# Kernel tuning notes

Measured on AMD Instinct MI355X. Metric: run time of the kernel, lower is better.

The kernel has to match this reference:

```python
import jax, jax.numpy as jnp
import numpy as np

TOP_K = 2
LORA_SCALE = 32.0 / 16.0  # alpha / r


def setup_inputs() -> dict:
    key = jax.random.key(0)
    ks = jax.random.split(key, 11)
    B, S, D, F, E, R = 4, 1024, 2048, 5632, 8, 16
    sd, sf = 1.0 / np.sqrt(D), 1.0 / np.sqrt(F)
    return {
        "x": jax.random.normal(ks[0], (B, S, D), jnp.float32),
        "gate_w": jax.random.normal(ks[1], (E, D), jnp.float32) * 0.02,
        "w1": jax.random.normal(ks[2], (F, D), jnp.float32) * sd,
        "w3": jax.random.normal(ks[3], (F, D), jnp.float32) * sd,
        "w2": jax.random.normal(ks[4], (D, F), jnp.float32) * sf,
        "a1": jax.random.normal(ks[5], (E, R, D), jnp.float32) * sd,
        "b1": jax.random.normal(ks[6], (E, F, R), jnp.float32) * 0.01,
        "a3": jax.random.normal(ks[7], (E, R, D), jnp.float32) * sd,
        "b3": jax.random.normal(ks[8], (E, F, R), jnp.float32) * 0.01,
        "a2": jax.random.normal(ks[9], (E, R, F), jnp.float32) * sf,
        "b2": jax.random.normal(ks[10], (E, D, R), jnp.float32) * 0.01,
    }


def reference(x, gate_w, w1, w3, w2, a1, b1, a3, b3, a2, b2):
    B, S, D = x.shape
    E = gate_w.shape[0]
    xf = x.reshape(B * S, D)                      # [N, D] tokens
    N = xf.shape[0]

    # Mixtral-style router: top-k over expert logits, softmax over selected.
    logits = xf @ gate_w.T                        # [N, E]
    top_w, top_i = jax.lax.top_k(logits, TOP_K)   # [N, k]
    routing = jax.nn.softmax(top_w, axis=-1)
    # Dense [N, E] routing-weight matrix (zero for unselected experts).
    w_full = jnp.zeros((N, E), x.dtype).at[jnp.arange(N)[:, None], top_i].add(routing)

    # Shared base up-projections computed once (same for every expert).
    base1 = xf @ w1.T                             # [N, F]
    base3 = xf @ w3.T                             # [N, F]

    def expert_step(acc, p):
        A1, B1, A3, B3, A2, B2, we = p            # we: [N] routing weight
        h1 = base1 + ((xf @ A1.T) @ B1.T) * LORA_SCALE
        h3 = base3 + ((xf @ A3.T) @ B3.T) * LORA_SCALE
        act = jax.nn.silu(h1) * h3                # SwiGLU, per-expert
        out = act @ w2.T + ((act @ A2.T) @ B2.T) * LORA_SCALE
        return acc + we[:, None] * out, None

    init = jnp.zeros((N, D), x.dtype)
    out, _ = jax.lax.scan(expert_step, init, (a1, b1, a3, b3, a2, b2, w_full.T))
    return out.reshape(B, S, D)
```

## Files before the change

### kernel.cpp

```cpp
#include <hip/hip_runtime.h>
#include <stdint.h>

#define NTOK 4096
#define DDIM 2048
#define FDIM 5632
#define NEXP 8
#define RLORA 16
#define TWOF 11264
#define BCOLS 11520
#define PADROWS 10240
#define LSCALE 2.0f

typedef __attribute__((ext_vector_type(4))) float f32x4;
typedef __attribute__((ext_vector_type(8))) short short8;
typedef unsigned short u16;

#define AS1 __attribute__((address_space(1)))
#define AS3 __attribute__((address_space(3)))

__device__ __forceinline__ float b2f(short s) {
  union { float f; unsigned u; } v;
  v.u = ((unsigned)(u16)s) << 16;
  return v.f;
}
__device__ __forceinline__ u16 f2b(float f) {
  union { float f; unsigned u; } v; v.f = f;
  unsigned r = v.u + 0x7fffu + ((v.u >> 16) & 1u);
  return (u16)(r >> 16);
}

__global__ __launch_bounds__(256) void cast_kernel(const float* __restrict__ src, u16* __restrict__ dst, int n4) {
  int stride = gridDim.x * 256;
  for (int i = blockIdx.x * 256 + threadIdx.x; i < n4; i += stride) {
    float4 v = reinterpret_cast<const float4*>(src)[i];
    ushort4 o;
    o.x = f2b(v.x); o.y = f2b(v.y); o.z = f2b(v.z); o.w = f2b(v.w);
    reinterpret_cast<ushort4*>(dst)[i] = o;
  }
}

__global__ __launch_bounds__(256) void cast_ball(const float* __restrict__ w1, const float* __restrict__ w3,
                                                 const float* __restrict__ a1, const float* __restrict__ a3,
                                                 u16* __restrict__ Ball) {
  const int n4 = BCOLS * DDIM / 4;
  int stride = gridDim.x * 256;
  for (int i = blockIdx.x * 256 + threadIdx.x; i < n4; i += stride) {
    int row = i >> 9;
    int c4 = i & 511;
    const float* src;
    if (row < FDIM)            src = w1 + (size_t)row * DDIM;
    else if (row < TWOF)       src = w3 + (size_t)(row - FDIM) * DDIM;
    else if (row < TWOF + 128) src = a1 + (size_t)(row - TWOF) * DDIM;
    else                       src = a3 + (size_t)(row - TWOF - 128) * DDIM;
    float4 v = reinterpret_cast<const float4*>(src)[c4];
    ushort4 o;
    o.x = f2b(v.x); o.y = f2b(v.y); o.z = f2b(v.z); o.w = f2b(v.w);
    reinterpret_cast<ushort4*>(Ball)[i] = o;
  }
}

__global__ __launch_bounds__(256) void router_cast(const float* __restrict__ x, const float* __restrict__ gw,
                                                   int2* __restrict__ tok_e, float2* __restrict__ tok_w,
                                                   u16* __restrict__ xb) {
  int tok = blockIdx.x;
  const float* xr = x + (size_t)tok * DDIM;
  int j0 = threadIdx.x * 8;
  float4 v0 = *reinterpret_cast<const float4*>(xr + j0);
  float4 v1 = *reinterpret_cast<const float4*>(xr + j0 + 4);
  float v[8] = {v0.x, v0.y, v0.z, v0.w, v1.x, v1.y, v1.z, v1.w};
  short8 ob;
#pragma unroll
  for (int j = 0; j < 8; ++j) ob[j] = (short)f2b(v[j]);
  *reinterpret_cast<short8*>(xb + (size_t)tok * DDIM + j0) = ob;
  float acc[NEXP];
#pragma unroll
  for (int e = 0; e < NEXP; ++e) {
    const float* gr = gw + e * DDIM + j0;
    float s = 0.f;
#pragma unroll
    for (int j = 0; j < 8; ++j) s += v[j] * gr[j];
    acc[e] = s;
  }
#pragma unroll
  for (int e = 0; e < NEXP; ++e) {
#pragma unroll
    for (int off = 32; off > 0; off >>= 1) acc[e] += __shfl_down(acc[e], off);
  }
  __shared__ float red[4][NEXP];
  int wid = threadIdx.x >> 6;
  int lane = threadIdx.x & 63;
  if (lane == 0) {
#pragma unroll
    for (int e = 0; e < NEXP; ++e) red[wid][e] = acc[e];
  }
  __syncthreads();
  if (threadIdx.x == 0) {
    float l[NEXP];
#pragma unroll
    for (int e = 0; e < NEXP; ++e) l[e] = red[0][e] + red[1][e] + red[2][e] + red[3][e];
    int i0 = 0;
#pragma unroll
    for (int e = 1; e < NEXP; ++e) if (l[e] > l[i0]) i0 = e;
    int i1 = (i0 == 0) ? 1 : 0;
#pragma unroll
    for (int e = 0; e < NEXP; ++e) if (e != i0 && e != i1 && l[e] > l[i1]) i1 = e;
    float ex = __expf(l[i1] - l[i0]);
    float w0 = 1.f / (1.f + ex);
    float w1v = ex / (1.f + ex);
    int2 ev; ev.x = i0; ev.y = i1;
    float2 wv; wv.x = w0; wv.y = w1v;
    tok_e[tok] = ev;
    tok_w[tok] = wv;
  }
}

__global__ __launch_bounds__(256) void build_pairs(const int2* __restrict__ tok_e,
                                                   int* __restrict__ pair_tok,
                                                   int* __restrict__ pair_k, int* __restrict__ poff) {
  __shared__ int cnt[NEXP];
  __shared__ int base[NEXP + 1];
  __shared__ int cur[NEXP];
  if (threadIdx.x < NEXP) cnt[threadIdx.x] = 0;
  __syncthreads();
  for (int t = threadIdx.x; t < NTOK; t += 256) {
    int2 ee = tok_e[t];
    atomicAdd(&cnt[ee.x], 1);
    atomicAdd(&cnt[ee.y], 1);
  }
  for (int i = threadIdx.x; i < PADROWS; i += 256) pair_tok[i] = -1;
  __syncthreads();
  if (threadIdx.x == 0) {
    int o = 0;
#pragma unroll
    for (int e = 0; e < NEXP; ++e) { base[e] = o; o += ((cnt[e] + 255) >> 8) << 8; }
    base[NEXP] = o;
  }
  __syncthreads();
  if (threadIdx.x < NEXP) cur[threadIdx.x] = base[threadIdx.x];
  __syncthreads();
  for (int t = threadIdx.x; t < NTOK; t += 256) {
    int2 ee = tok_e[t];
    int s0 = atomicAdd(&cur[ee.x], 1);
    pair_tok[s0] = t; pair_k[s0] = 0;
    int s1 = atomicAdd(&cur[ee.y], 1);
    pair_tok[s1] = t; pair_k[s1] = 1;
  }
  __syncthreads();
  if (threadIdx.x <= NEXP) poff[threadIdx.x] = base[threadIdx.x];
}

__device__ __forceinline__ void stage64(const u16* __restrict__ src, int ld, char* ldsb, int tid) {
#pragma unroll
  for (int h = 0; h < 4; ++h) {
    int q = h * 256 + tid;
    int r = q >> 3, g = q & 7;
    int gs = g ^ (r & 7);
    const char* s = (const char*)(src + (size_t)r * ld) + gs * 16;
    __builtin_amdgcn_global_load_lds((const AS1 void*)s, (AS3 void*)(ldsb + q * 16), 16, 0, 0);
  }
}

__device__ __forceinline__ void mm128(const u16* __restrict__ A, const u16* __restrict__ B,
                                      int lda, int ldb, int NT,
                                      char* lA, char* lB, int tid,
                                      int rowAb, int rowBb, int col0,
                                      f32x4 (&acc)[4][4]) {
  for (int t = 0; t < NT; ++t) {
    __syncthreads();
    stage64(A + (size_t)t * 64, lda, lA, tid);
    stage64(B + (size_t)t * 64, ldb, lB, tid);
    __syncthreads();
    short8 av[4], bv[4];
#pragma unroll
    for (int kh = 0; kh < 2; ++kh) {
      int col = col0 ^ (kh << 6);
#pragma unroll
      for (int i = 0; i < 4; ++i) {
        av[i] = *(const short8*)(lA + rowAb + i * 2048 + col);
        bv[i] = *(const short8*)(lB + rowBb + i * 2048 + col);
      }
#pragma unroll
      for (int i = 0; i < 4; ++i)
#pragma unroll
        for (int j = 0; j < 4; ++j)
          acc[i][j] = __builtin_amdgcn_mfma_f32_16x16x32_bf16(av[i], bv[j], acc[i][j], 0, 0, 0);
    }
  }
}

__global__ __launch_bounds__(256, 4) void gemm_base(const u16* __restrict__ xb, const u16* __restrict__ Ball,
                                                    u16* __restrict__ base13) {
  __shared__ char lA[16384];
  __shared__ char lB[16384];
  const int tid = threadIdx.x;
  const int lane = tid & 63, wid = tid >> 6;
  const int wr = wid >> 1, wc = wid & 1;
  const int lm = lane & 15, lg = lane >> 4;
  const int col0 = (lg << 4) ^ ((lm & 7) << 4);
  const int rowAb = (wr * 64 + lm) * 128;
  const int rowBb = (wc * 64 + lm) * 128;
  const int lq = (lane >> 4) << 2;
  int orig = blockIdx.x;
  int wgid = (orig & 7) * 360 + (orig >> 3);
  int mi = wgid & 31, nt = wgid >> 5;
  int m0 = mi << 7, n0 = nt << 7;
  f32x4 acc[4][4];
  f32x4 z = {0.f, 0.f, 0.f, 0.f};
#pragma unroll
  for (int i = 0; i < 4; ++i)
#pragma unroll
    for (int j = 0; j < 4; ++j) acc[i][j] = z;
  mm128(xb + (size_t)m0 * DDIM, Ball + (size_t)n0 * DDIM, DDIM, DDIM, DDIM / 64,
        lA, lB, tid, rowAb, rowBb, col0, acc);
#pragma unroll
  for (int i = 0; i < 4; ++i) {
#pragma unroll
    for (int n = 0; n < 4; ++n) {
      int col = n0 + wc * 64 + n * 16 + lm;
#pragma unroll
      for (int q = 0; q < 4; ++q) {
        int row = m0 + wr * 64 + i * 16 + lq + q;
        base13[(size_t)row * BCOLS + col] = f2b(acc[i][n][q]);
      }
    }
  }
}

__global__ __launch_bounds__(256) void act_kernel(const u16* __restrict__ base13,
                                                  const float* __restrict__ b1, const float* __restrict__ b3,
                                                  const int* __restrict__ pair_tok, const int* __restrict__ poff,
                                                  u16* __restrict__ act) {
  __shared__ float lb1[128 * 16];
  __shared__ float lb3[128 * 16];
  int f0 = blockIdx.x * 128;
  int r0 = blockIdx.y * 32;
  if (r0 >= poff[NEXP]) return;
  int e = 0;
  while (r0 >= poff[e + 1]) ++e;
  const float4* pb1 = reinterpret_cast<const float4*>(b1 + ((size_t)e * FDIM + f0) * RLORA);
  const float4* pb3 = reinterpret_cast<const float4*>(b3 + ((size_t)e * FDIM + f0) * RLORA);
  for (int i = threadIdx.x; i < 128 * 16 / 4; i += 256) {
    int r = i >> 2, c = i & 3;
    int cs = (c + (r >> 5)) & 3;
    *reinterpret_cast<float4*>(lb1 + r * 16 + cs * 4) = pb1[i];
    *reinterpret_cast<float4*>(lb3 + r * 16 + cs * 4) = pb3[i];
  }
  __syncthreads();
  int pr = r0 + (threadIdx.x >> 3);
  int fg = (threadIdx.x & 7) << 4;
  int tok = pair_tok[pr];
  if (tok < 0) return;
  const u16* bp = base13 + (size_t)tok * BCOLS;
  short8 x1a = *(const short8*)(bp + TWOF + e * 16);
  short8 x1b = *(const short8*)(bp + TWOF + e * 16 + 8);
  short8 x3a = *(const short8*)(bp + TWOF + NEXP * RLORA + e * 16);
  short8 x3b = *(const short8*)(bp + TWOF + NEXP * RLORA + e * 16 + 8);
  float xa1[16], xa3[16];
#pragma unroll
  for (int r = 0; r < 8; ++r) {
    xa1[r] = b2f(x1a[r]); xa1[r + 8] = b2f(x1b[r]);
    xa3[r] = b2f(x3a[r]); xa3[r + 8] = b2f(x3b[r]);
  }
  short8 h1a = *(const short8*)(bp + f0 + fg);
  short8 h1b = *(const short8*)(bp + f0 + fg + 8);
  short8 h3a = *(const short8*)(bp + FDIM + f0 + fg);
  short8 h3b = *(const short8*)(bp + FDIM + f0 + fg + 8);
  short8 o0, o1;
#pragma unroll
  for (int ii = 0; ii < 16; ++ii) {
    float hb1 = b2f(ii < 8 ? h1a[ii] : h1b[ii - 8]);
    float hb3 = b2f(ii < 8 ? h3a[ii] : h3b[ii - 8]);
    int row = fg + ii;
    int rot = row >> 5;
    const float* l1 = lb1 + row * 16;
    const float* l3 = lb3 + row * 16;
    float d1 = 0.f, d3 = 0.f;
#pragma unroll
    for (int c = 0; c < 4; ++c) {
      int cs = ((c + rot) & 3) << 2;
      float4 v1 = *reinterpret_cast<const float4*>(l1 + cs);
      float4 v3 = *reinterpret_cast<const float4*>(l3 + cs);
      d1 += xa1[4 * c + 0] * v1.x + xa1[4 * c + 1] * v1.y + xa1[4 * c + 2] * v1.z + xa1[4 * c + 3] * v1.w;
      d3 += xa3[4 * c + 0] * v3.x + xa3[4 * c + 1] * v3.y + xa3[4 * c + 2] * v3.z + xa3[4 * c + 3] * v3.w;
    }
    float h1 = hb1 + LSCALE * d1;
    float h3 = hb3 + LSCALE * d3;
    float s = h1 / (1.f + __expf(-h1));
    u16 ob = f2b(s * h3);
    if (ii < 8) o0[ii] = (short)ob; else o1[ii - 8] = (short)ob;
  }
  short8* dst = (short8*)(act + (size_t)pr * FDIM + f0 + fg);
  dst[0] = o0;
  dst[1] = o1;
}

__global__ __launch_bounds__(256) void ya2_kernel(const u16* __restrict__ act, const float* __restrict__ a2,
                                                  const int* __restrict__ poff, float* __restrict__ ya2) {
  __shared__ float lact[16 * 68];
  __shared__ float la2[16 * 68];
  int r0 = blockIdx.x * 16;
  if (r0 >= poff[NEXP]) return;
  int e = 0;
  while (r0 >= poff[e + 1]) ++e;
  int p = threadIdx.x >> 4;
  int r = threadIdx.x & 15;
  int lrow = threadIdx.x >> 4;
  int c4 = (threadIdx.x & 15) << 2;
  float acc = 0.f;
  for (int f0 = 0; f0 < FDIM; f0 += 64) {
    __syncthreads();
    ushort4 av = *reinterpret_cast<const ushort4*>(act + (size_t)(r0 + lrow) * FDIM + f0 + c4);
    lact[lrow * 68 + c4 + 0] = b2f((short)av.x);
    lact[lrow * 68 + c4 + 1] = b2f((short)av.y);
    lact[lrow * 68 + c4 + 2] = b2f((short)av.z);
    lact[lrow * 68 + c4 + 3] = b2f((short)av.w);
    float4 bv = *reinterpret_cast<const float4*>(a2 + ((size_t)e * RLORA + lrow) * FDIM + f0 + c4);
    *reinterpret_cast<float4*>(la2 + lrow * 68 + c4) = bv;
    __syncthreads();
#pragma unroll
    for (int jj = 0; jj < 64; jj += 4) {
      float4 a4 = *reinterpret_cast<const float4*>(lact + p * 68 + jj);
      float4 b4 = *reinterpret_cast<const float4*>(la2 + r * 68 + jj);
      acc += a4.x * b4.x + a4.y * b4.y + a4.z * b4.z + a4.w * b4.w;
    }
  }
  ya2[(size_t)(r0 + p) * RLORA + r] = acc;
}

__global__ __launch_bounds__(256, 4) void gemm_down(const u16* __restrict__ act, const u16* __restrict__ w2b,
                                                    const float* __restrict__ b2, const float* __restrict__ ya2,
                                                    const int* __restrict__ pair_tok, const int* __restrict__ pair_k,
                                                    const int* __restrict__ poff,
                                                    float* __restrict__ slots) {
  int orig = blockIdx.x;
  int wgid = (orig & 7) * 160 + (orig >> 3);
  int nt = wgid & 15;
  int miL = wgid >> 4;
  int mi = ((miL % 10) << 3) + (miL / 10);
  int m0 = mi << 7;
  if (m0 >= poff[NEXP]) return;
  int e = 0;
  while (m0 >= poff[e + 1]) ++e;
  int n0 = nt << 7;
  __shared__ char lA[16384];
  __shared__ char lB[16384];
  const int tid = threadIdx.x;
  const int lane = tid & 63, wid = tid >> 6;
  const int wr = wid >> 1, wc = wid & 1;
  const int lm = lane & 15, lg = lane >> 4;
  const int col0 = (lg << 4) ^ ((lm & 7) << 4);
  const int rowAb = (wr * 64 + lm) * 128;
  const int rowBb = (wc * 64 + lm) * 128;
  const int lq = (lane >> 4) << 2;
  f32x4 acc[4][4];
  f32x4 z = {0.f, 0.f, 0.f, 0.f};
#pragma unroll
  for (int i = 0; i < 4; ++i)
#pragma unroll
    for (int j = 0; j < 4; ++j) acc[i][j] = z;
  mm128(act + (size_t)m0 * FDIM, w2b + (size_t)n0 * FDIM, FDIM, FDIM, FDIM / 64,
        lA, lB, tid, rowAb, rowBb, col0, acc);
#pragma unroll
  for (int n = 0; n < 4; ++n) {
    int col = n0 + wc * 64 + n * 16 + lm;
    const float* b2p = b2 + ((size_t)e * DDIM + col) * RLORA;
    float b2v[16];
#pragma unroll
    for (int rr = 0; rr < 16; ++rr) b2v[rr] = b2p[rr];
#pragma unroll
    for (int i = 0; i < 4; ++i) {
#pragma unroll
      for (int q = 0; q < 4; ++q) {
        int pidx = m0 + wr * 64 + i * 16 + lq + q;
        int tok = pair_tok[pidx];
        if (tok < 0) continue;
        const float* yr = ya2 + (size_t)pidx * RLORA;
        float dot = 0.f;
#pragma unroll
        for (int rr = 0; rr < 16; ++rr) dot += yr[rr] * b2v[rr];
        slots[((size_t)tok * 2 + pair_k[pidx]) * DDIM + col] = acc[i][n][q] + LSCALE * dot;
      }
    }
  }
}

__global__ __launch_bounds__(256) void combine_kernel(const float4* __restrict__ slots,
                                                      const float2* __restrict__ tok_w,
                                                      float4* __restrict__ out) {
  const int n4 = NTOK * (DDIM / 4);
  int stride = gridDim.x * 256;
  for (int i = blockIdx.x * 256 + threadIdx.x; i < n4; i += stride) {
    int tok = i >> 9;
    int c = i & 511;
    float2 w = tok_w[tok];
    float4 v0 = slots[(size_t)(tok * 2) * 512 + c];
    float4 v1 = slots[(size_t)(tok * 2 + 1) * 512 + c];
    float4 o;
    o.x = w.x * v0.x + w.y * v1.x;
    o.y = w.x * v0.y + w.y * v1.y;
    o.z = w.x * v0.z + w.y * v1.z;
    o.w = w.x * v0.w + w.y * v1.w;
    out[i] = o;
  }
}

extern "C" void kernel_launch(void* const* d_in, const int* in_sizes, int n_in,
                              void* d_out, int out_size, void* d_ws, size_t ws_size,
                              hipStream_t stream) {
  (void)in_sizes; (void)n_in; (void)out_size; (void)ws_size;
  const float* x  = (const float*)d_in[0];
  const float* gw = (const float*)d_in[1];
  const float* w1 = (const float*)d_in[2];
  const float* w3 = (const float*)d_in[3];
  const float* w2 = (const float*)d_in[4];
  const float* a1 = (const float*)d_in[5];
  const float* b1 = (const float*)d_in[6];
  const float* a3 = (const float*)d_in[7];
  const float* b3 = (const float*)d_in[8];
  const float* a2 = (const float*)d_in[9];
  const float* b2 = (const float*)d_in[10];
  float* out = (float*)d_out;

  char* ws = (char*)d_ws;
  size_t off = 0;
  auto take = [&](size_t bytes) -> char* {
    char* p = ws + off;
    off += (bytes + 255) & ~(size_t)255;
    return p;
  };
  char* reg1 = take((size_t)NTOK * BCOLS * 2);
  u16* base13 = (u16*)reg1;
  float* slots = (float*)reg1;
  float* ya2 = (float*)(reg1 + (size_t)NTOK * 2 * DDIM * 4);
  char* reg2 = take((size_t)PADROWS * FDIM * 2);
  u16* actb = (u16*)reg2;
  u16* xb = (u16*)reg2;
  u16* Ball = (u16*)(reg2 + (size_t)NTOK * DDIM * 2);
  u16* w2b = (u16*)take((size_t)DDIM * FDIM * 2);
  int2* tok_e   = (int2*)take((size_t)NTOK * 8);
  float2* tok_w = (float2*)take((size_t)NTOK * 8);
  int* pair_tok = (int*)take((size_t)PADROWS * 4);
  int* pair_k   = (int*)take((size_t)PADROWS * 4);
  int* poff     = (int*)take(256);

  cast_ball<<<2048, 256, 0, stream>>>(w1, w3, a1, a3, Ball);
  cast_kernel<<<1024, 256, 0, stream>>>(w2, w2b, DDIM * FDIM / 4);
  router_cast<<<NTOK, 256, 0, stream>>>(x, gw, tok_e, tok_w, xb);
  build_pairs<<<1, 256, 0, stream>>>(tok_e, pair_tok, pair_k, poff);
  gemm_base<<<2880, 256, 0, stream>>>(xb, Ball, base13);
  dim3 g3(FDIM / 128, PADROWS / 32);
  act_kernel<<<g3, 256, 0, stream>>>(base13, b1, b3, pair_tok, poff, actb);
  ya2_kernel<<<PADROWS / 16, 256, 0, stream>>>(actb, a2, poff, ya2);
  gemm_down<<<1280, 256, 0, stream>>>(actb, w2b, b2, ya2, pair_tok, pair_k, poff, slots);
  combine_kernel<<<2048, 256, 0, stream>>>((const float4*)slots, tok_w, (float4*)out);
}
```

Measured before the change: 853.9 us.

## Rewrite LoRA down-projection A2 kernel with bf16 MFMA and split-K atomics

The ya2 kernel, which computes act times A2 transposed for each routed row, moves from scalar fp32 LDS dot products to bf16 MFMA 16x16x32. It loads swizzled tiles straight into LDS with global_load_lds, and uses 64-row tiles with the F dimension split across two blocks. Partial sums are combined with atomicAdd into a buffer that is zeroed first, and A2 gets an extra bf16 cast pass. This cuts the ALU and LDS cost of a reduction over a long K, at the price of a memset, atomics and lower A2 precision.

```diff
diff --git a/kernel.cpp b/kernel.cpp
--- a/kernel.cpp
+++ b/kernel.cpp
@@ -294,37 +294,50 @@
   dst[1] = o1;
 }
 
-__global__ __launch_bounds__(256) void ya2_kernel(const u16* __restrict__ act, const float* __restrict__ a2,
+__global__ __launch_bounds__(256) void ya2_kernel(const u16* __restrict__ act, const u16* __restrict__ a2b,
                                                   const int* __restrict__ poff, float* __restrict__ ya2) {
-  __shared__ float lact[16 * 68];
-  __shared__ float la2[16 * 68];
-  int r0 = blockIdx.x * 16;
-  if (r0 >= poff[NEXP]) return;
+  __shared__ char lA[8192];
+  __shared__ char lB[2048];
+  int m0 = blockIdx.x * 64;
+  if (m0 >= poff[NEXP]) return;
   int e = 0;
-  while (r0 >= poff[e + 1]) ++e;
-  int p = threadIdx.x >> 4;
-  int r = threadIdx.x & 15;
-  int lrow = threadIdx.x >> 4;
-  int c4 = (threadIdx.x & 15) << 2;
-  float acc = 0.f;
-  for (int f0 = 0; f0 < FDIM; f0 += 64) {
+  while (m0 >= poff[e + 1]) ++e;
+  int f0 = blockIdx.y * (FDIM / 2);
+  const int tid = threadIdx.x;
+  const int lane = tid & 63, w = tid >> 6;
+  const int lm = lane & 15, lg = lane >> 4;
+  const int col0 = (lg << 4) ^ ((lm & 7) << 4);
+  const int rowAb = (w * 16 + lm) * 128;
+  const int rowBb = lm * 128;
+  const int lq = (lane >> 4) << 2;
+  const u16* A = act + (size_t)m0 * FDIM + f0;
+  const u16* B = a2b + (size_t)e * RLORA * FDIM + f0;
+  f32x4 acc = {0.f, 0.f, 0.f, 0.f};
+  for (int t = 0; t < FDIM / 128; ++t) {
     __syncthreads();
-    ushort4 av = *reinterpret_cast<const ushort4*>(act + (size_t)(r0 + lrow) * FDIM + f0 + c4);
-    lact[lrow * 68 + c4 + 0] = b2f((short)av.x);
-    lact[lrow * 68 + c4 + 1] = b2f((short)av.y);
-    lact[lrow * 68 + c4 + 2] = b2f((short)av.z);
-    lact[lrow * 68 + c4 + 3] = b2f((short)av.w);
-    float4 bv = *reinterpret_cast<const float4*>(a2 + ((size_t)e * RLORA + lrow) * FDIM + f0 + c4);
-    *reinterpret_cast<float4*>(la2 + lrow * 68 + c4) = bv;
+#pragma unroll
+    for (int h = 0; h < 2; ++h) {
+      int q = h * 256 + tid, r = q >> 3, g = q & 7, gs = g ^ (r & 7);
+      const char* s = (const char*)(A + (size_t)t * 64 + (size_t)r * FDIM) + gs * 16;
+      __builtin_amdgcn_global_load_lds((const AS1 void*)s, (AS3 void*)(lA + q * 16), 16, 0, 0);
+    }
+    if (tid < 128) {
+      int q = tid, r = q >> 3, g = q & 7, gs = g ^ (r & 7);
+      const char* s = (const char*)(B + (size_t)t * 64 + (size_t)r * FDIM) + gs * 16;
+      __builtin_amdgcn_global_load_lds((const AS1 void*)s, (AS3 void*)(lB + q * 16), 16, 0, 0);
+    }
     __syncthreads();
 #pragma unroll
-    for (int jj = 0; jj < 64; jj += 4) {
-      float4 a4 = *reinterpret_cast<const float4*>(lact + p * 68 + jj);
-      float4 b4 = *reinterpret_cast<const float4*>(la2 + r * 68 + jj);
-      acc += a4.x * b4.x + a4.y * b4.y + a4.z * b4.z + a4.w * b4.w;
-    }
-  }
-  ya2[(size_t)(r0 + p) * RLORA + r] = acc;
+    for (int kh = 0; kh < 2; ++kh) {
+      int col = col0 ^ (kh << 6);
+      short8 av = *(const short8*)(lA + rowAb + col);
+      short8 bv = *(const short8*)(lB + rowBb + col);
+      acc = __builtin_amdgcn_mfma_f32_16x16x32_bf16(av, bv, acc, 0, 0, 0);
+    }
+  }
+#pragma unroll
+  for (int q = 0; q < 4; ++q)
+    atomicAdd(&ya2[(size_t)(m0 + w * 16 + lq + q) * RLORA + lm], acc[q]);
 }
 
 __global__ __launch_bounds__(256, 4) void gemm_down(const u16* __restrict__ act, const u16* __restrict__ w2b,
@@ -431,12 +444,13 @@
   char* reg1 = take((size_t)NTOK * BCOLS * 2);
   u16* base13 = (u16*)reg1;
   float* slots = (float*)reg1;
-  float* ya2 = (float*)(reg1 + (size_t)NTOK * 2 * DDIM * 4);
   char* reg2 = take((size_t)PADROWS * FDIM * 2);
   u16* actb = (u16*)reg2;
   u16* xb = (u16*)reg2;
   u16* Ball = (u16*)(reg2 + (size_t)NTOK * DDIM * 2);
   u16* w2b = (u16*)take((size_t)DDIM * FDIM * 2);
+  u16* a2b = (u16*)take((size_t)NEXP * RLORA * FDIM * 2);
+  float* ya2 = (float*)take((size_t)PADROWS * RLORA * 4);
   int2* tok_e   = (int2*)take((size_t)NTOK * 8);
   float2* tok_w = (float2*)take((size_t)NTOK * 8);
   int* pair_tok = (int*)take((size_t)PADROWS * 4);
@@ -445,12 +459,15 @@
 
   cast_ball<<<2048, 256, 0, stream>>>(w1, w3, a1, a3, Ball);
   cast_kernel<<<1024, 256, 0, stream>>>(w2, w2b, DDIM * FDIM / 4);
+  cast_kernel<<<64, 256, 0, stream>>>(a2, a2b, NEXP * RLORA * FDIM / 4);
   router_cast<<<NTOK, 256, 0, stream>>>(x, gw, tok_e, tok_w, xb);
   build_pairs<<<1, 256, 0, stream>>>(tok_e, pair_tok, pair_k, poff);
   gemm_base<<<2880, 256, 0, stream>>>(xb, Ball, base13);
   dim3 g3(FDIM / 128, PADROWS / 32);
   act_kernel<<<g3, 256, 0, stream>>>(base13, b1, b3, pair_tok, poff, actb);
-  ya2_kernel<<<PADROWS / 16, 256, 0, stream>>>(actb, a2, poff, ya2);
+  hipMemsetAsync(ya2, 0, (size_t)PADROWS * RLORA * 4, stream);
+  dim3 gy(PADROWS / 64, 2);
+  ya2_kernel<<<gy, 256, 0, stream>>>(actb, a2b, poff, ya2);
   gemm_down<<<1280, 256, 0, stream>>>(actb, w2b, b2, ya2, pair_tok, pair_k, poff, slots);
   combine_kernel<<<2048, 256, 0, stream>>>((const float4*)slots, tok_w, (float4*)out);
 }
```

After: 776.7 us, median of 2. 1.1x faster.
